# Kernel tuning notes

Hardware: AMD Instinct MI355X
Metric: run time of the kernel (lower is better)

## Reference

```python
import jax, jax.numpy as jnp
import numpy as np
import math

B, S, DIM = 1, 2048, 1024
H, KVH = 16, 4
HD = DIM // H            # 64
KV_DIM = KVH * HD        # 256


def setup_inputs() -> dict:
    key = jax.random.key(0)
    ks = jax.random.split(key, 8)
    std = 0.02
    return {
        "x": jax.random.normal(ks[0], (B, S, DIM), jnp.float32),
        "Wq": jax.random.normal(ks[1], (DIM, DIM), jnp.float32) * std,
        "Wk": jax.random.normal(ks[2], (KV_DIM, DIM), jnp.float32) * std,
        "Wv": jax.random.normal(ks[3], (KV_DIM, DIM), jnp.float32) * std,
        "Wg": jax.random.normal(ks[4], (KV_DIM, DIM), jnp.float32) * std,
        "Wo": jax.random.normal(ks[5], (DIM, DIM), jnp.float32) * std,
        "q_gain": jnp.full((H,), 1.0, jnp.float32),
        "lambda_param": jnp.full((H,), 0.5, jnp.float32),
    }


def _rms_norm(x):
    eps = jnp.finfo(x.dtype).eps
    return x * jax.lax.rsqrt(jnp.mean(x * x, axis=-1, keepdims=True) + eps)


def _polar_rotary(seq_len, head_dim, dtype):
    # PolarRotary: angles = arange(0, d, 2)/d * pi; radius decays with position
    angles = jnp.arange(0, head_dim, 2, dtype=jnp.float32) / head_dim * math.pi
    pos = jnp.arange(seq_len, dtype=jnp.float32)
    radius = 1.0 / (1.0 + pos[:, None] * 0.01)          # [S, 1]
    ang = pos[:, None] * angles[None, :]                 # [S, d/2]
    cos = (radius * jnp.cos(ang)).astype(dtype)          # [S, d/2]
    sin = (radius * jnp.sin(ang)).astype(dtype)
    return cos[None, None], sin[None, None]              # [1,1,S,d/2]


def _apply_rotary(x, cos, sin):
    half = x.shape[-1] // 2
    x1, x2 = x[..., :half], x[..., half:]
    return jnp.concatenate([x1 * cos + x2 * sin, x1 * -sin + x2 * cos], axis=-1)


def _causal_attn(q, k, v, scale, mask):
    # q,k,v: [B,H,S,d]
    s = jnp.einsum("bhqd,bhkd->bhqk", q, k) * scale
    s = jnp.where(mask, s, jnp.finfo(s.dtype).min)
    p = jax.nn.softmax(s, axis=-1)
    return jnp.einsum("bhqk,bhkd->bhqd", p, v)


def reference(x, Wq, Wk, Wv, Wg, Wo, q_gain, lambda_param):
    bsz, seqlen, dim = x.shape
    q = (x @ Wq.T).reshape(bsz, seqlen, H, HD).transpose(0, 2, 1, 3)      # [B,H,S,d]
    k = (x @ Wk.T).reshape(bsz, seqlen, KVH, HD).transpose(0, 2, 1, 3)    # [B,KVH,S,d]
    v = (x @ Wv.T).reshape(bsz, seqlen, KVH, HD).transpose(0, 2, 1, 3)

    # value gate (VGA)
    v_g = jax.nn.sigmoid((x @ Wg.T).reshape(bsz, seqlen, KVH, HD).transpose(0, 2, 1, 3))
    v = v * v_g

    q = _rms_norm(q)
    k = _rms_norm(k)

    cos, sin = _polar_rotary(seqlen, HD, q.dtype)
    q = _apply_rotary(q, cos, sin)
    k = _apply_rotary(k, cos, sin)

    q = q * q_gain.astype(q.dtype)[None, :, None, None]

    # GQA: repeat kv heads
    rep = H // KVH
    k = jnp.repeat(k, rep, axis=1)
    v = jnp.repeat(v, rep, axis=1)

    # differential attention: split head dim in halves
    half = HD // 2
    q1, q2 = q[..., :half], q[..., half:]
    k1, k2 = k[..., :half], k[..., half:]
    v1, v2 = v[..., :half], v[..., half:]

    scale = 1.0 / math.sqrt(half)
    mask = jnp.tril(jnp.ones((seqlen, seqlen), dtype=bool))[None, None]
    a1 = _causal_attn(q1, k1, v1, scale, mask)
    a2 = _causal_attn(q2, k2, v2, scale, mask)

    lp = lambda_param.astype(q.dtype)[None, :, None, None]
    y = jnp.concatenate([a1 - lp * a2, a1 + lp * a2], axis=-1)            # [B,H,S,d]
    y = y.transpose(0, 2, 1, 3).reshape(bsz, seqlen, dim)
    return y @ Wo.T
```

## Files before the change

### kernel.cpp

```cpp
#include <hip/hip_runtime.h>
#include <hip/hip_bf16.h>
#include <math.h>

#define S_LEN 2048
#define DIM   1024
#define NH    16
#define NKVH  4
#define HD    64
#define KVDIM 256

typedef __hip_bfloat16 bf16;
typedef __attribute__((ext_vector_type(8))) short short8;
typedef __attribute__((ext_vector_type(4))) float f32x4;

#define GLOBAL_AS __attribute__((address_space(1)))
#define LDS_AS    __attribute__((address_space(3)))

__device__ __forceinline__ void gload_lds16(const bf16* g, bf16* l) {
    __builtin_amdgcn_global_load_lds((const GLOBAL_AS void*)g, (LDS_AS void*)l,
                                     16, 0, 0);
}

__global__ __launch_bounds__(256) void cast6(
    const float* __restrict__ x,  const float* __restrict__ Wq,
    const float* __restrict__ Wk, const float* __restrict__ Wv,
    const float* __restrict__ Wg, const float* __restrict__ Wo,
    bf16* __restrict__ xb,  bf16* __restrict__ Wqb,
    bf16* __restrict__ Wkb, bf16* __restrict__ Wvb,
    bf16* __restrict__ Wgb, bf16* __restrict__ Wob,
    float* __restrict__ rc, float* __restrict__ rs) {
    if (blockIdx.y == 6) {
        const int idx = blockIdx.x * 256 + threadIdx.x;
        if (idx < S_LEN * 32) {
            const int s = idx >> 5, i = idx & 31;
            float af  = (float)(((double)(2 * i) / 64.0) * 3.14159265358979323846);
            float ang = (float)s * af;
            float radius = 1.0f / (1.0f + 0.01f * (float)s);
            rc[idx] = radius * (float)cos((double)ang);
            rs[idx] = radius * (float)sin((double)ang);
        }
        return;
    }
    const float* s; bf16* d; int n;
    switch (blockIdx.y) {
        case 0: s = x;  d = xb;  n = S_LEN * DIM; break;
        case 1: s = Wq; d = Wqb; n = DIM * DIM;   break;
        case 2: s = Wk; d = Wkb; n = KVDIM * DIM; break;
        case 3: s = Wv; d = Wvb; n = KVDIM * DIM; break;
        case 4: s = Wg; d = Wgb; n = KVDIM * DIM; break;
        default: s = Wo; d = Wob; n = DIM * DIM;  break;
    }
    for (int i = (blockIdx.x * 256 + threadIdx.x) * 4; i < n; i += gridDim.x * 1024) {
        float4 v = *(const float4*)(s + i);
        d[i]     = __float2bfloat16(v.x);
        d[i + 1] = __float2bfloat16(v.y);
        d[i + 2] = __float2bfloat16(v.z);
        d[i + 3] = __float2bfloat16(v.w);
    }
}

__device__ __forceinline__ void gemm_core(
    const bf16* __restrict__ A, const bf16* __restrict__ B,
    float* __restrict__ C, int bm, int bn, int N, int K) {
    __shared__ bf16 As[64 * 64];
    __shared__ bf16 Bs[64 * 64];
    const int tid  = threadIdx.x;
    const int w    = tid >> 6;
    const int lane = tid & 63;
    const int quad = lane >> 4;
    const int lm   = lane & 15;
    const int srow = tid >> 3;
    const int sseg = (tid & 7) ^ (srow & 7);
    const bf16* a0p = A + (size_t)(bm + srow) * K + (sseg << 3);
    const bf16* a1p = a0p + (size_t)32 * K;
    const bf16* b0p = B + (size_t)(bn + srow) * K + (sseg << 3);
    const bf16* b1p = b0p + (size_t)32 * K;
    bf16* ldsA = As + w * 512;
    bf16* ldsB = Bs + w * 512;

    f32x4 acc[4] = {};
    const int ra  = w * 16 + lm;
    const int rax = ra & 7;
    const int aoff0 = ra * 64 + (((quad    ) ^ rax) << 3);
    const int aoff1 = ra * 64 + (((quad + 4) ^ rax) << 3);
    const int rbx = lm & 7;
    const int boff0 = lm * 64 + (((quad    ) ^ rbx) << 3);
    const int boff1 = lm * 64 + (((quad + 4) ^ rbx) << 3);

    for (int k0 = 0; k0 < K; k0 += 64) {
        gload_lds16(a0p + k0, ldsA);
        gload_lds16(a1p + k0, ldsA + 2048);
        gload_lds16(b0p + k0, ldsB);
        gload_lds16(b1p + k0, ldsB + 2048);
        __syncthreads();
        short8 a0 = *(const short8*)&As[aoff0];
        short8 a1 = *(const short8*)&As[aoff1];
        #pragma unroll
        for (int t = 0; t < 4; ++t) {
            short8 b0 = *(const short8*)&Bs[boff0 + t * 16 * 64];
            short8 b1 = *(const short8*)&Bs[boff1 + t * 16 * 64];
            acc[t] = __builtin_amdgcn_mfma_f32_16x16x32_bf16(a0, b0, acc[t], 0, 0, 0);
            acc[t] = __builtin_amdgcn_mfma_f32_16x16x32_bf16(a1, b1, acc[t], 0, 0, 0);
        }
        __syncthreads();
    }
    const int r0 = bm + w * 16 + quad * 4;
    #pragma unroll
    for (int t = 0; t < 4; ++t) {
        const int col = bn + t * 16 + lm;
        #pragma unroll
        for (int i = 0; i < 4; ++i)
            C[(size_t)(r0 + i) * N + col] = acc[t][i];
    }
}

__global__ __launch_bounds__(256) void gemm_qkvg(
    const bf16* __restrict__ xb, const bf16* __restrict__ Wqb,
    const bf16* __restrict__ Wkb, const bf16* __restrict__ Wvb,
    const bf16* __restrict__ Wgb, float* __restrict__ Qp,
    float* __restrict__ KVG) {
    const int c0 = blockIdx.x * 64;
    const bf16* B; float* C; int bn, N;
    if (c0 < DIM) { B = Wqb; C = Qp; bn = c0; N = DIM; }
    else {
        const int t = c0 - DIM;
        const int wsel = t >> 8;
        B = (wsel == 0) ? Wkb : (wsel == 1) ? Wvb : Wgb;
        C = KVG + (size_t)wsel * S_LEN * KVDIM;
        bn = t & 255; N = KVDIM;
    }
    gemm_core(xb, B, C, blockIdx.y * 64, bn, N, DIM);
}

__global__ __launch_bounds__(256) void gemm_out(
    const bf16* __restrict__ Yb, const bf16* __restrict__ Wob,
    float* __restrict__ C) {
    gemm_core(Yb, Wob, C, blockIdx.y * 64, blockIdx.x * 64, DIM, DIM);
}

__device__ __forceinline__ float rms_rot_val(
    const float* __restrict__ p, int s, int lane, float gain,
    const float* __restrict__ rc, const float* __restrict__ rs) {
    float x = p[lane];
    float ss = x * x;
    #pragma unroll
    for (int o = 32; o > 0; o >>= 1) ss += __shfl_xor(ss, o);
    float n = x * rsqrtf(ss * (1.0f/64.0f) + 1.1920928955078125e-7f);
    float other = __shfl_xor(n, 32);
    int i = lane & 31;
    float c  = rc[s * 32 + i];
    float sn = rs[s * 32 + i];
    return (n * c + ((lane < 32) ? other * sn : -other * sn)) * gain;
}

__global__ __launch_bounds__(64) void postproc_pk(
    const float* __restrict__ Qp, const float* __restrict__ Kp,
    const float* __restrict__ Vp, const float* __restrict__ Gp,
    bf16* __restrict__ Qb, bf16* __restrict__ Kpk, bf16* __restrict__ Vpk,
    const float* __restrict__ qgain,
    const float* __restrict__ rc, const float* __restrict__ rs) {
    const int s = blockIdx.x;
    const int unit = blockIdx.y;
    const int lane = threadIdx.x;
    const int half = lane >> 5, d32 = lane & 31;
    const int kb = s >> 5;
    if (unit < NH) {
        float v = rms_rot_val(Qp + (size_t)s * DIM + unit * HD, s, lane, qgain[unit], rc, rs);
        Qb[(size_t)s * DIM + unit * HD + lane] = __float2bfloat16(v);
    } else if (unit < NH + NKVH) {
        const int kvh = unit - NH;
        float v = rms_rot_val(Kp + (size_t)s * KVDIM + kvh * HD, s, lane, 1.0f, rc, rs);
        const size_t ki = (((((size_t)(kvh*2 + half)*64 + kb)*2 + ((s&31)>>4))*64)
                           + (d32>>3)*16 + (s&15))*8 + (d32&7);
        Kpk[ki] = __float2bfloat16(v);
    } else {
        const int kvh = unit - NH - NKVH;
        const float* v = Vp + (size_t)s * KVDIM + kvh * HD;
        const float* g = Gp + (size_t)s * KVDIM + kvh * HD;
        float gv = g[lane];
        float val = v[lane] / (1.0f + __expf(-gv));
        const size_t vi = (((((size_t)(kvh*2 + half)*64 + kb)*2 + (d32>>4))*64)
                           + ((s&31)>>3)*16 + (d32&15))*8 + (s&7);
        Vpk[vi] = __float2bfloat16(val);
    }
}

__global__ __launch_bounds__(64, 4) void attn_mfma(
    const bf16* __restrict__ Qb, const bf16* __restrict__ Kpk,
    const bf16* __restrict__ Vpk, float* __restrict__ Ao) {
    __shared__ short PW[640];
    const int id    = blockIdx.x;
    const int qtile = 127 - (id >> 5);
    const int hh    = id & 31;
    const int h     = hh >> 1;
    const int half  = hh & 1;
    const int kvh   = h >> 2;
    const int lane  = threadIdx.x;
    const int quad  = lane >> 4;
    const int m     = lane & 15;
    bf16* PWb = (bf16*)PW;

    const int qrow = qtile * 16 + m;
    short8 qf = *(const short8*)(Qb + (size_t)qrow * DIM + h * HD + half * 32 + quad * 8);

    const bf16* kbase = Kpk + (size_t)(kvh * 2 + half) * 64 * 1024 + lane * 8;
    const bf16* vbase = Vpk + (size_t)(kvh * 2 + half) * 64 * 1024 + lane * 8;

    f32x4 o0 = {}, o1 = {};
    float lpart[4] = {0.f, 0.f, 0.f, 0.f};
    const float scale = 0.17677669529663687f;
    const int rbase = qtile * 16 + quad * 4;
    const int nkt = (qtile >> 1) + 1;

    for (int kb = 0; kb < nkt; ++kb) {
        short8 kf0 = *(const short8*)(kbase + kb * 1024);
        short8 kf1 = *(const short8*)(kbase + kb * 1024 + 512);
        f32x4 s0 = {}, s1 = {};
        s0 = __builtin_amdgcn_mfma_f32_16x16x32_bf16(qf, kf0, s0, 0, 0, 0);
        s1 = __builtin_amdgcn_mfma_f32_16x16x32_bf16(qf, kf1, s1, 0, 0, 0);
        short8 vtf0 = *(const short8*)(vbase + kb * 1024);
        short8 vtf1 = *(const short8*)(vbase + kb * 1024 + 512);
        const int kg = kb * 32 + m;
        #pragma unroll
        for (int r = 0; r < 4; ++r) {
            const int rg = rbase + r;
            const float p0 = (kg > rg)      ? 0.f : __expf(s0[r] * scale);
            const float p1 = (kg + 16 > rg) ? 0.f : __expf(s1[r] * scale);
            lpart[r] += p0 + p1;
            PWb[(quad * 4 + r) * 40 + m]      = __float2bfloat16(p0);
            PWb[(quad * 4 + r) * 40 + 16 + m] = __float2bfloat16(p1);
        }
        asm volatile("s_waitcnt lgkmcnt(0)" ::: "memory");
        short8 pf = *(const short8*)&PW[m * 40 + quad * 8];
        o0 = __builtin_amdgcn_mfma_f32_16x16x32_bf16(pf, vtf0, o0, 0, 0, 0);
        o1 = __builtin_amdgcn_mfma_f32_16x16x32_bf16(pf, vtf1, o1, 0, 0, 0);
    }

    #pragma unroll
    for (int r = 0; r < 4; ++r) {
        float v = lpart[r];
        v += __shfl_xor(v, 1);
        v += __shfl_xor(v, 2);
        v += __shfl_xor(v, 4);
        v += __shfl_xor(v, 8);
        lpart[r] = 1.f / v;
    }
    #pragma unroll
    for (int r = 0; r < 4; ++r) {
        float* op = Ao + (size_t)(rbase + r) * DIM + h * HD + half * 32;
        op[m]      = o0[r] * lpart[r];
        op[16 + m] = o1[r] * lpart[r];
    }
}

__global__ __launch_bounds__(256) void combine_kernel(
    const float* __restrict__ A, const float* __restrict__ lambda_p,
    bf16* __restrict__ Y) {
    const int idx = blockIdx.x * 256 + threadIdx.x;
    const int c = idx & (DIM - 1);
    const int s = idx >> 10;
    const int hh = c >> 6;
    const int d = c & 63;
    const float* base = A + (size_t)s * DIM + hh * HD;
    const float lam = lambda_p[hh];
    float y;
    if (d < 32) y = base[d]      - lam * base[d + 32];
    else        y = base[d - 32] + lam * base[d];
    Y[idx] = __float2bfloat16(y);
}

extern "C" void kernel_launch(void* const* d_in, const int* in_sizes, int n_in,
                              void* d_out, int out_size, void* d_ws, size_t ws_size,
                              hipStream_t stream) {
    const float* x  = (const float*)d_in[0];
    const float* Wq = (const float*)d_in[1];
    const float* Wk = (const float*)d_in[2];
    const float* Wv = (const float*)d_in[3];
    const float* Wg = (const float*)d_in[4];
    const float* Wo = (const float*)d_in[5];
    const float* qg = (const float*)d_in[6];
    const float* lp = (const float*)d_in[7];
    float* out = (float*)d_out;

    char* ws = (char*)d_ws;
    float* Qp  = (float*)(ws);
    float* KVG = (float*)(ws + (8u  << 20));
    float* Kp  = KVG;
    float* Vp  = KVG + (size_t)S_LEN * KVDIM;
    float* Gp  = KVG + (size_t)2 * S_LEN * KVDIM;
    float* Ao  = (float*)(ws + (14u << 20));
    float* rc  = (float*)(ws + (14u << 20));
    float* rs  = (float*)(ws + (14u << 20) + (256u << 10));
    bf16* xb   = (bf16*)(ws + (22u << 20));
    bf16* Wqb  = (bf16*)(ws + (26u << 20));
    bf16* Wkb  = (bf16*)(ws + (28u << 20));
    bf16* Wvb  = (bf16*)(ws + (28u << 20) + (512u << 10));
    bf16* Wgb  = (bf16*)(ws + (29u << 20));
    bf16* Wob  = (bf16*)(ws + (29u << 20) + (512u << 10));
    bf16* Qb   = (bf16*)(ws + (22u << 20));
    bf16* Kpk  = (bf16*)(ws + (26u << 20));
    bf16* Vpk  = (bf16*)(ws + (27u << 20));
    bf16* Yb   = (bf16*)ws;

    cast6<<<dim3(512, 7), 256, 0, stream>>>(x, Wq, Wk, Wv, Wg, Wo,
                                            xb, Wqb, Wkb, Wvb, Wgb, Wob, rc, rs);

    gemm_qkvg<<<dim3(28, S_LEN/64), 256, 0, stream>>>(xb, Wqb, Wkb, Wvb, Wgb, Qp, KVG);

    postproc_pk<<<dim3(S_LEN, NH + 2*NKVH), 64, 0, stream>>>(
        Qp, Kp, Vp, Gp, Qb, Kpk, Vpk, qg, rc, rs);

    attn_mfma<<<4096, 64, 0, stream>>>(Qb, Kpk, Vpk, Ao);

    combine_kernel<<<S_LEN * DIM / 256, 256, 0, stream>>>(Ao, lp, Yb);

    gemm_out<<<dim3(DIM/64, S_LEN/64), 256, 0, stream>>>(Yb, Wob, out);
}
```

Before: 162.2 us.

## Enlarge GEMM tiles to 128x128 and 128x64 with 2x2 warp layout

Replaces the 64x64 GEMM core with a templated core that uses 128-row tiles and a 2x2 wave layout, each wave computing a 4xNREP grid of 16x16 MFMA outputs over a K-step of 32. The QKVG projection uses 128x128 tiles and the output projection uses 128x64 tiles, with the launch grids shrunk to match. The aim is more MFMA work per LDS load and fewer global reloads of A and B tiles. In exchange the K-step halves, so there are twice as many barriers, the LDS swizzle is dropped (which may add bank conflicts), register use rises, and fewer blocks are launched.

```diff
diff --git a/kernel.cpp b/kernel.cpp
--- a/kernel.cpp
+++ b/kernel.cpp
@@ -59,58 +59,69 @@
     }
 }
 
-__device__ __forceinline__ void gemm_core(
+template<int MREP, int NREP>
+__device__ __forceinline__ void gemm_core128(
     const bf16* __restrict__ A, const bf16* __restrict__ B,
     float* __restrict__ C, int bm, int bn, int N, int K) {
-    __shared__ bf16 As[64 * 64];
-    __shared__ bf16 Bs[64 * 64];
+    constexpr int BM = MREP * 32;
+    constexpr int BN = NREP * 32;
+    __shared__ bf16 As[BM * 32];
+    __shared__ bf16 Bs[BN * 32];
     const int tid  = threadIdx.x;
     const int w    = tid >> 6;
     const int lane = tid & 63;
     const int quad = lane >> 4;
     const int lm   = lane & 15;
-    const int srow = tid >> 3;
-    const int sseg = (tid & 7) ^ (srow & 7);
-    const bf16* a0p = A + (size_t)(bm + srow) * K + (sseg << 3);
-    const bf16* a1p = a0p + (size_t)32 * K;
-    const bf16* b0p = B + (size_t)(bn + srow) * K + (sseg << 3);
-    const bf16* b1p = b0p + (size_t)32 * K;
-    bf16* ldsA = As + w * 512;
-    bf16* ldsB = Bs + w * 512;
-
-    f32x4 acc[4] = {};
-    const int ra  = w * 16 + lm;
-    const int rax = ra & 7;
-    const int aoff0 = ra * 64 + (((quad    ) ^ rax) << 3);
-    const int aoff1 = ra * 64 + (((quad + 4) ^ rax) << 3);
-    const int rbx = lm & 7;
-    const int boff0 = lm * 64 + (((quad    ) ^ rbx) << 3);
-    const int boff1 = lm * 64 + (((quad + 4) ^ rbx) << 3);
-
-    for (int k0 = 0; k0 < K; k0 += 64) {
-        gload_lds16(a0p + k0, ldsA);
-        gload_lds16(a1p + k0, ldsA + 2048);
-        gload_lds16(b0p + k0, ldsB);
-        gload_lds16(b1p + k0, ldsB + 2048);
+    const int wr   = w >> 1, wc = w & 1;
+    const int srow = tid >> 2;
+    const int scol = (tid & 3) << 3;
+    const bf16* aSrc = A + (size_t)(bm + srow) * K + scol;
+    const bf16* bSrc = B + (size_t)(bn + srow) * K + scol;
+    bf16* aDst = As + w * 512;
+    bf16* bDst = Bs + w * 512;
+    constexpr int ALOADS = BM / 64;
+    constexpr int BLOADS = BN / 64;
+
+    f32x4 acc[MREP][NREP] = {};
+    int aoff[MREP], boff[NREP];
+    #pragma unroll
+    for (int m = 0; m < MREP; ++m)
+        aoff[m] = (wr * (16 * MREP) + m * 16 + lm) * 32 + quad * 8;
+    #pragma unroll
+    for (int n = 0; n < NREP; ++n)
+        boff[n] = (wc * (16 * NREP) + n * 16 + lm) * 32 + quad * 8;
+
+    for (int k0 = 0; k0 < K; k0 += 32) {
+        #pragma unroll
+        for (int i = 0; i < ALOADS; ++i)
+            gload_lds16(aSrc + (size_t)(i * 64) * K + k0, aDst + i * 2048);
+        #pragma unroll
+        for (int i = 0; i < BLOADS; ++i)
+            gload_lds16(bSrc + (size_t)(i * 64) * K + k0, bDst + i * 2048);
         __syncthreads();
-        short8 a0 = *(const short8*)&As[aoff0];
-        short8 a1 = *(const short8*)&As[aoff1];
-        #pragma unroll
-        for (int t = 0; t < 4; ++t) {
-            short8 b0 = *(const short8*)&Bs[boff0 + t * 16 * 64];
-            short8 b1 = *(const short8*)&Bs[boff1 + t * 16 * 64];
-            acc[t] = __builtin_amdgcn_mfma_f32_16x16x32_bf16(a0, b0, acc[t], 0, 0, 0);
-            acc[t] = __builtin_amdgcn_mfma_f32_16x16x32_bf16(a1, b1, acc[t], 0, 0, 0);
+        short8 af[MREP], bfr[NREP];
+        #pragma unroll
+        for (int m = 0; m < MREP; ++m) af[m]  = *(const short8*)&As[aoff[m]];
+        #pragma unroll
+        for (int n = 0; n < NREP; ++n) bfr[n] = *(const short8*)&Bs[boff[n]];
+        #pragma unroll
+        for (int m = 0; m < MREP; ++m)
+            #pragma unroll
+            for (int n = 0; n < NREP; ++n)
+                acc[m][n] = __builtin_amdgcn_mfma_f32_16x16x32_bf16(
+                    af[m], bfr[n], acc[m][n], 0, 0, 0);
+        __syncthreads();
+    }
+    #pragma unroll
+    for (int m = 0; m < MREP; ++m) {
+        const int r0 = bm + wr * (16 * MREP) + m * 16 + quad * 4;
+        #pragma unroll
+        for (int n = 0; n < NREP; ++n) {
+            const int col = bn + wc * (16 * NREP) + n * 16 + lm;
+            #pragma unroll
+            for (int i = 0; i < 4; ++i)
+                C[(size_t)(r0 + i) * N + col] = acc[m][n][i];
         }
-        __syncthreads();
-    }
-    const int r0 = bm + w * 16 + quad * 4;
-    #pragma unroll
-    for (int t = 0; t < 4; ++t) {
-        const int col = bn + t * 16 + lm;
-        #pragma unroll
-        for (int i = 0; i < 4; ++i)
-            C[(size_t)(r0 + i) * N + col] = acc[t][i];
     }
 }
 
@@ -119,23 +130,23 @@
     const bf16* __restrict__ Wkb, const bf16* __restrict__ Wvb,
     const bf16* __restrict__ Wgb, float* __restrict__ Qp,
     float* __restrict__ KVG) {
-    const int c0 = blockIdx.x * 64;
+    const int cx = blockIdx.x;
     const bf16* B; float* C; int bn, N;
-    if (c0 < DIM) { B = Wqb; C = Qp; bn = c0; N = DIM; }
+    if (cx < 8) { B = Wqb; C = Qp; bn = cx * 128; N = DIM; }
     else {
-        const int t = c0 - DIM;
-        const int wsel = t >> 8;
+        const int t = cx - 8;
+        const int wsel = t >> 1;
         B = (wsel == 0) ? Wkb : (wsel == 1) ? Wvb : Wgb;
         C = KVG + (size_t)wsel * S_LEN * KVDIM;
-        bn = t & 255; N = KVDIM;
-    }
-    gemm_core(xb, B, C, blockIdx.y * 64, bn, N, DIM);
+        bn = (t & 1) * 128; N = KVDIM;
+    }
+    gemm_core128<4, 4>(xb, B, C, blockIdx.y * 128, bn, N, DIM);
 }
 
 __global__ __launch_bounds__(256) void gemm_out(
     const bf16* __restrict__ Yb, const bf16* __restrict__ Wob,
     float* __restrict__ C) {
-    gemm_core(Yb, Wob, C, blockIdx.y * 64, blockIdx.x * 64, DIM, DIM);
+    gemm_core128<4, 2>(Yb, Wob, C, blockIdx.y * 128, blockIdx.x * 64, DIM, DIM);
 }
 
 __device__ __forceinline__ float rms_rot_val(
@@ -305,7 +316,7 @@
     cast6<<<dim3(512, 7), 256, 0, stream>>>(x, Wq, Wk, Wv, Wg, Wo,
                                             xb, Wqb, Wkb, Wvb, Wgb, Wob, rc, rs);
 
-    gemm_qkvg<<<dim3(28, S_LEN/64), 256, 0, stream>>>(xb, Wqb, Wkb, Wvb, Wgb, Qp, KVG);
+    gemm_qkvg<<<dim3(14, S_LEN/128), 256, 0, stream>>>(xb, Wqb, Wkb, Wvb, Wgb, Qp, KVG);
 
     postproc_pk<<<dim3(S_LEN, NH + 2*NKVH), 64, 0, stream>>>(
         Qp, Kp, Vp, Gp, Qb, Kpk, Vpk, qg, rc, rs);
@@ -314,5 +325,5 @@
 
     combine_kernel<<<S_LEN * DIM / 256, 256, 0, stream>>>(Ao, lp, Yb);
 
-    gemm_out<<<dim3(DIM/64, S_LEN/64), 256, 0, stream>>>(Yb, Wob, out);
-}
+    gemm_out<<<dim3(DIM/64, S_LEN/128), 256, 0, stream>>>(Yb, Wob, out);
+}
```

New measurement: 176.6 us. 8.8% more time.

## Fuse QKVG projection GEMM with RMS-norm, rotary, gating and packing epilogue

Applied to the files above, without the earlier changes.

Merges the QKV/gate projection GEMM and the separate postprocessing kernel into one kernel. The GEMM epilogue now applies RMS norm, polar rotary, q_gain, sigmoid value gating and packed-layout bf16 stores straight from the MFMA accumulators. V and G tiles share the A tile within one block, which computes both products together. This removes the fp32 Q/K/V/G intermediate round trip through global memory and one launch. The cost is an uneven per-block workload, since gate blocks do twice the MFMA work, and scattered packed stores from the epilogue.

```diff
diff --git a/kernel.cpp b/kernel.cpp
--- a/kernel.cpp
+++ b/kernel.cpp
@@ -114,74 +114,142 @@
     }
 }
 
-__global__ __launch_bounds__(256) void gemm_qkvg(
-    const bf16* __restrict__ xb, const bf16* __restrict__ Wqb,
-    const bf16* __restrict__ Wkb, const bf16* __restrict__ Wvb,
-    const bf16* __restrict__ Wgb, float* __restrict__ Qp,
-    float* __restrict__ KVG) {
-    const int c0 = blockIdx.x * 64;
-    const bf16* B; float* C; int bn, N;
-    if (c0 < DIM) { B = Wqb; C = Qp; bn = c0; N = DIM; }
-    else {
-        const int t = c0 - DIM;
-        const int wsel = t >> 8;
-        B = (wsel == 0) ? Wkb : (wsel == 1) ? Wvb : Wgb;
-        C = KVG + (size_t)wsel * S_LEN * KVDIM;
-        bn = t & 255; N = KVDIM;
-    }
-    gemm_core(xb, B, C, blockIdx.y * 64, bn, N, DIM);
-}
-
 __global__ __launch_bounds__(256) void gemm_out(
     const bf16* __restrict__ Yb, const bf16* __restrict__ Wob,
     float* __restrict__ C) {
     gemm_core(Yb, Wob, C, blockIdx.y * 64, blockIdx.x * 64, DIM, DIM);
 }
 
-__device__ __forceinline__ float rms_rot_val(
-    const float* __restrict__ p, int s, int lane, float gain,
-    const float* __restrict__ rc, const float* __restrict__ rs) {
-    float x = p[lane];
-    float ss = x * x;
-    #pragma unroll
-    for (int o = 32; o > 0; o >>= 1) ss += __shfl_xor(ss, o);
-    float n = x * rsqrtf(ss * (1.0f/64.0f) + 1.1920928955078125e-7f);
-    float other = __shfl_xor(n, 32);
-    int i = lane & 31;
-    float c  = rc[s * 32 + i];
-    float sn = rs[s * 32 + i];
-    return (n * c + ((lane < 32) ? other * sn : -other * sn)) * gain;
-}
-
-__global__ __launch_bounds__(64) void postproc_pk(
-    const float* __restrict__ Qp, const float* __restrict__ Kp,
-    const float* __restrict__ Vp, const float* __restrict__ Gp,
+__global__ __launch_bounds__(256) void gemm_qkvg_post(
+    const bf16* __restrict__ xb,  const bf16* __restrict__ Wqb,
+    const bf16* __restrict__ Wkb, const bf16* __restrict__ Wvb,
+    const bf16* __restrict__ Wgb,
     bf16* __restrict__ Qb, bf16* __restrict__ Kpk, bf16* __restrict__ Vpk,
     const float* __restrict__ qgain,
     const float* __restrict__ rc, const float* __restrict__ rs) {
-    const int s = blockIdx.x;
-    const int unit = blockIdx.y;
-    const int lane = threadIdx.x;
-    const int half = lane >> 5, d32 = lane & 31;
-    const int kb = s >> 5;
-    if (unit < NH) {
-        float v = rms_rot_val(Qp + (size_t)s * DIM + unit * HD, s, lane, qgain[unit], rc, rs);
-        Qb[(size_t)s * DIM + unit * HD + lane] = __float2bfloat16(v);
-    } else if (unit < NH + NKVH) {
-        const int kvh = unit - NH;
-        float v = rms_rot_val(Kp + (size_t)s * KVDIM + kvh * HD, s, lane, 1.0f, rc, rs);
-        const size_t ki = (((((size_t)(kvh*2 + half)*64 + kb)*2 + ((s&31)>>4))*64)
-                           + (d32>>3)*16 + (s&15))*8 + (d32&7);
-        Kpk[ki] = __float2bfloat16(v);
+    __shared__ bf16 As[64 * 64];
+    __shared__ bf16 Bs[64 * 64];
+    __shared__ bf16 Gs[64 * 64];
+    const int cx = blockIdx.x;
+    const int bm = blockIdx.y * 64;
+    const int tid  = threadIdx.x;
+    const int w    = tid >> 6;
+    const int lane = tid & 63;
+    const int quad = lane >> 4;
+    const int lm   = lane & 15;
+    const int srow = tid >> 3;
+    const int sseg = (tid & 7) ^ (srow & 7);
+
+    int mode, bn;
+    const bf16 *B0, *B1;
+    if (cx < 4)      { mode = 2; bn = cx * 64;        B0 = Wvb; B1 = Wgb; }
+    else if (cx < 8) { mode = 1; bn = (cx - 4) * 64;  B0 = Wkb; B1 = Wkb; }
+    else             { mode = 0; bn = (cx - 8) * 64;  B0 = Wqb; B1 = Wqb; }
+
+    const bf16* a0p = xb + (size_t)(bm + srow) * DIM + (sseg << 3);
+    const bf16* a1p = a0p + (size_t)32 * DIM;
+    const bf16* b0p = B0 + (size_t)(bn + srow) * DIM + (sseg << 3);
+    const bf16* b1p = b0p + (size_t)32 * DIM;
+    const bf16* g0p = B1 + (size_t)(bn + srow) * DIM + (sseg << 3);
+    const bf16* g1p = g0p + (size_t)32 * DIM;
+    bf16* ldsA = As + w * 512;
+    bf16* ldsB = Bs + w * 512;
+    bf16* ldsG = Gs + w * 512;
+
+    f32x4 acc[4]  = {};
+    f32x4 acc2[4] = {};
+    const int ra  = w * 16 + lm;
+    const int rax = ra & 7;
+    const int aoff0 = ra * 64 + (((quad    ) ^ rax) << 3);
+    const int aoff1 = ra * 64 + (((quad + 4) ^ rax) << 3);
+    const int rbx = lm & 7;
+    const int boff0 = lm * 64 + (((quad    ) ^ rbx) << 3);
+    const int boff1 = lm * 64 + (((quad + 4) ^ rbx) << 3);
+
+    for (int k0 = 0; k0 < DIM; k0 += 64) {
+        gload_lds16(a0p + k0, ldsA);
+        gload_lds16(a1p + k0, ldsA + 2048);
+        gload_lds16(b0p + k0, ldsB);
+        gload_lds16(b1p + k0, ldsB + 2048);
+        if (mode == 2) {
+            gload_lds16(g0p + k0, ldsG);
+            gload_lds16(g1p + k0, ldsG + 2048);
+        }
+        __syncthreads();
+        short8 a0 = *(const short8*)&As[aoff0];
+        short8 a1 = *(const short8*)&As[aoff1];
+        #pragma unroll
+        for (int t = 0; t < 4; ++t) {
+            short8 b0 = *(const short8*)&Bs[boff0 + t * 16 * 64];
+            short8 b1 = *(const short8*)&Bs[boff1 + t * 16 * 64];
+            acc[t] = __builtin_amdgcn_mfma_f32_16x16x32_bf16(a0, b0, acc[t], 0, 0, 0);
+            acc[t] = __builtin_amdgcn_mfma_f32_16x16x32_bf16(a1, b1, acc[t], 0, 0, 0);
+        }
+        if (mode == 2) {
+            #pragma unroll
+            for (int t = 0; t < 4; ++t) {
+                short8 g0 = *(const short8*)&Gs[boff0 + t * 16 * 64];
+                short8 g1 = *(const short8*)&Gs[boff1 + t * 16 * 64];
+                acc2[t] = __builtin_amdgcn_mfma_f32_16x16x32_bf16(a0, g0, acc2[t], 0, 0, 0);
+                acc2[t] = __builtin_amdgcn_mfma_f32_16x16x32_bf16(a1, g1, acc2[t], 0, 0, 0);
+            }
+        }
+        __syncthreads();
+    }
+
+    const int r0 = bm + w * 16 + quad * 4;
+    if (mode == 2) {
+        const int kvh = cx;
+        #pragma unroll
+        for (int t = 0; t < 4; ++t) {
+            const int d = t * 16 + lm;
+            const int half = d >> 5, d32 = d & 31;
+            #pragma unroll
+            for (int i = 0; i < 4; ++i) {
+                const int s = r0 + i;
+                float val = acc[t][i] / (1.0f + __expf(-acc2[t][i]));
+                const size_t vi = (((((size_t)(kvh*2 + half)*64 + (s>>5))*2 + (d32>>4))*64)
+                                   + ((s&31)>>3)*16 + (d32&15))*8 + (s&7);
+                Vpk[vi] = __float2bfloat16(val);
+            }
+        }
     } else {
-        const int kvh = unit - NH - NKVH;
-        const float* v = Vp + (size_t)s * KVDIM + kvh * HD;
-        const float* g = Gp + (size_t)s * KVDIM + kvh * HD;
-        float gv = g[lane];
-        float val = v[lane] / (1.0f + __expf(-gv));
-        const size_t vi = (((((size_t)(kvh*2 + half)*64 + kb)*2 + (d32>>4))*64)
-                           + ((s&31)>>3)*16 + (d32&15))*8 + (s&7);
-        Vpk[vi] = __float2bfloat16(val);
+        const float gain = (mode == 0) ? qgain[cx - 8] : 1.0f;
+        float rr[4];
+        #pragma unroll
+        for (int i = 0; i < 4; ++i) {
+            float v0 = acc[0][i] * acc[0][i] + acc[2][i] * acc[2][i];
+            float v1 = acc[1][i] * acc[1][i] + acc[3][i] * acc[3][i];
+            float ssv = v0 + v1;
+            ssv += __shfl_xor(ssv, 8);
+            ssv += __shfl_xor(ssv, 4);
+            ssv += __shfl_xor(ssv, 2);
+            ssv += __shfl_xor(ssv, 1);
+            rr[i] = rsqrtf(ssv * (1.0f/64.0f) + 1.1920928955078125e-7f);
+        }
+        #pragma unroll
+        for (int t = 0; t < 4; ++t) {
+            const int d = t * 16 + lm;
+            #pragma unroll
+            for (int i = 0; i < 4; ++i) {
+                const int s = r0 + i;
+                float n  = acc[t][i]     * rr[i];
+                float no = acc[t ^ 2][i] * rr[i];
+                const int ri = s * 32 + (d & 31);
+                float c = rc[ri], sn = rs[ri];
+                float val = (t < 2) ? (n * c + no * sn) * gain
+                                    : (n * c + -no * sn) * gain;
+                if (mode == 0) {
+                    Qb[(size_t)s * DIM + (cx - 8) * 64 + d] = __float2bfloat16(val);
+                } else {
+                    const int kvh = cx - 4;
+                    const int half = d >> 5, d32 = d & 31;
+                    const size_t ki = (((((size_t)(kvh*2 + half)*64 + (s>>5))*2 + ((s&31)>>4))*64)
+                                       + (d32>>3)*16 + (s&15))*8 + (d32&7);
+                    Kpk[ki] = __float2bfloat16(val);
+                }
+            }
+        }
     }
 }
 
@@ -283,32 +351,25 @@
     float* out = (float*)d_out;
 
     char* ws = (char*)d_ws;
-    float* Qp  = (float*)(ws);
-    float* KVG = (float*)(ws + (8u  << 20));
-    float* Kp  = KVG;
-    float* Vp  = KVG + (size_t)S_LEN * KVDIM;
-    float* Gp  = KVG + (size_t)2 * S_LEN * KVDIM;
-    float* Ao  = (float*)(ws + (14u << 20));
+    bf16* Qb   = (bf16*)ws;
+    bf16* Kpk  = (bf16*)(ws + (8u << 20));
+    bf16* Vpk  = (bf16*)(ws + (9u << 20));
     float* rc  = (float*)(ws + (14u << 20));
     float* rs  = (float*)(ws + (14u << 20) + (256u << 10));
+    float* Ao  = (float*)(ws + (14u << 20));
     bf16* xb   = (bf16*)(ws + (22u << 20));
     bf16* Wqb  = (bf16*)(ws + (26u << 20));
     bf16* Wkb  = (bf16*)(ws + (28u << 20));
     bf16* Wvb  = (bf16*)(ws + (28u << 20) + (512u << 10));
     bf16* Wgb  = (bf16*)(ws + (29u << 20));
     bf16* Wob  = (bf16*)(ws + (29u << 20) + (512u << 10));
-    bf16* Qb   = (bf16*)(ws + (22u << 20));
-    bf16* Kpk  = (bf16*)(ws + (26u << 20));
-    bf16* Vpk  = (bf16*)(ws + (27u << 20));
     bf16* Yb   = (bf16*)ws;
 
     cast6<<<dim3(512, 7), 256, 0, stream>>>(x, Wq, Wk, Wv, Wg, Wo,
                                             xb, Wqb, Wkb, Wvb, Wgb, Wob, rc, rs);
 
-    gemm_qkvg<<<dim3(28, S_LEN/64), 256, 0, stream>>>(xb, Wqb, Wkb, Wvb, Wgb, Qp, KVG);
-
-    postproc_pk<<<dim3(S_LEN, NH + 2*NKVH), 64, 0, stream>>>(
-        Qp, Kp, Vp, Gp, Qb, Kpk, Vpk, qg, rc, rs);
+    gemm_qkvg_post<<<dim3(24, S_LEN/64), 256, 0, stream>>>(
+        xb, Wqb, Wkb, Wvb, Wgb, Qb, Kpk, Vpk, qg, rc, rs);
 
     attn_mfma<<<4096, 64, 0, stream>>>(Qb, Kpk, Vpk, Ao);
 
```

New measurement: 149.3 us. -8.0%, faster.
